# Kernel tuning notes

Measured on AMD Instinct MI355X. Metric: run time of the kernel, lower is better.

Reference implementation:

```python
import jax, jax.numpy as jnp
import numpy as np

B, D_IN, D_FEAT, N_EX, N_LAB = 4096, 512, 512, 20000, 100
P_FACTOR = 3.0
EPS = 1e-12  # torch F.normalize eps


def setup_inputs() -> dict:
    key = jax.random.key(0)
    k1, k2, k3, k4 = jax.random.split(key, 4)
    features = jax.random.normal(k1, (B, D_IN), dtype=jnp.float32)
    g_weight = jax.random.normal(k2, (D_FEAT, D_IN), dtype=jnp.float32) * (1.0 / np.sqrt(D_IN))
    ex_features = jax.random.normal(k3, (N_EX, D_IN), dtype=jnp.float32)
    ex_classes = jax.random.uniform(k4, (N_EX, N_LAB), dtype=jnp.float32)
    class_reps = jnp.eye(N_LAB, dtype=jnp.float32)  # one_hot(arange(num_labels)) since class_dim is None
    return {"features": features, "g_weight": g_weight, "ex_features": ex_features,
            "ex_classes": ex_classes, "class_reps": class_reps}


def _l2_normalize(x):
    n = jnp.linalg.norm(x, axis=-1, keepdims=True)
    return x / jnp.maximum(n, EPS)


def _l1_normalize(x):
    n = jnp.sum(jnp.abs(x), axis=-1, keepdims=True)
    return x / jnp.maximum(n, EPS)


def reference(features, g_weight, ex_features, ex_classes, class_reps):
    # g projection (bias-free linear)
    f = features @ g_weight.T          # [B, D_FEAT]
    e = ex_features @ g_weight.T       # [N_EX, D_FEAT]
    # exemplar class representations
    ex_class_reps = _l1_normalize(ex_classes) @ class_reps  # [N_EX, N_LAB]
    # cosine similarity
    s = _l2_normalize(f) @ _l2_normalize(e).T  # [B, N_EX]
    # power-sign activation then L1 row-normalize
    a = jnp.sign(s) * jnp.abs(s) ** P_FACTOR
    a = _l1_normalize(a)
    echo = a @ ex_class_reps           # [B, N_LAB]
    return echo
```

## Files before the change

kernel.cpp:

```cpp
#include <hip/hip_runtime.h>

#define B_ROWS 4096
#define D      512
#define N_EX   20000
#define EXP2   20096
#define MPROJ  24192
#define N_LAB  100
#define LABP2  128
#define NT2    157
#define SPLITS 16

typedef __attribute__((ext_vector_type(8)))  short short8v;
typedef __attribute__((ext_vector_type(16))) float f32x16;
typedef __attribute__((ext_vector_type(2)))  int   int2v;
typedef unsigned short u16;

__device__ __forceinline__ u16 f2bf(float x) {
    unsigned u = __builtin_bit_cast(unsigned, x);
    u = u + 0x7FFFu + ((u >> 16) & 1u);
    return (u16)(u >> 16);
}
__device__ __forceinline__ float bf2f(u16 h) {
    unsigned u = ((unsigned)h) << 16;
    return __builtin_bit_cast(float, u);
}

__device__ __forceinline__ void gload16(const void* g, void* l) {
    __builtin_amdgcn_global_load_lds((const __attribute__((address_space(1))) void*)g,
                                     (__attribute__((address_space(3))) void*)l, 16, 0, 0);
}

__device__ __forceinline__ unsigned pk_bf16(float a, float b) {
    unsigned r;
    asm("v_cvt_pk_bf16_f32 %0, %1, %2" : "=v"(r) : "v"(a), "v"(b));
    return r;
}

__device__ __forceinline__ void swap_halves(unsigned &a, unsigned &b) {
#if __has_builtin(__builtin_amdgcn_permlane32_swap)
    int2v r = __builtin_amdgcn_permlane32_swap((int)a, (int)b, false, false);
    a = (unsigned)r[0]; b = (unsigned)r[1];
#else
    unsigned sa = (unsigned)__shfl_xor((int)a, 32, 64);
    unsigned sb = (unsigned)__shfl_xor((int)b, 32, 64);
    if (threadIdx.x & 32) a = sb; else b = sa;
#endif
}

#define MFMA32(a, b, c) __builtin_amdgcn_mfma_f32_32x32x16_bf16((a), (b), (c), 0, 0, 0)

__global__ __launch_bounds__(256)
void split3_k(const float* __restrict__ f, const float* __restrict__ ex,
              const float* __restrict__ gw, u16* __restrict__ xall,
              u16* __restrict__ wh) {
    int i8 = blockIdx.x * 256 + threadIdx.x;
    int row = i8 >> 6;
    int e = (i8 & 63) * 8;
    const float* src = nullptr;
    u16* dst;
    if (row < B_ROWS) {
        src = &f[(size_t)row * D + e];
        dst = &xall[(size_t)row * D + e];
    } else if (row < B_ROWS + EXP2) {
        int er = row - B_ROWS;
        if (er < N_EX) src = &ex[(size_t)er * D + e];
        dst = &xall[(size_t)row * D + e];
    } else if (row < B_ROWS + EXP2 + D) {
        int wr = row - B_ROWS - EXP2;
        src = &gw[(size_t)wr * D + e];
        dst = &wh[(size_t)wr * D + e];
    } else return;
    short8v h = {0,0,0,0,0,0,0,0};
    if (src) {
        float4 a = *(const float4*)src, b = *(const float4*)(src + 4);
        float v[8] = {a.x,a.y,a.z,a.w,b.x,b.y,b.z,b.w};
        #pragma unroll
        for (int j = 0; j < 8; ++j) h[j] = (short)f2bf(v[j]);
    }
    *(short8v*)dst = h;
}

__global__ __launch_bounds__(512, 4)
void gemm128_k(const u16* __restrict__ A, const u16* __restrict__ B,
               u16* __restrict__ C) {
    __shared__ u16 BUF[2][128][128];
    const int tid = threadIdx.x;
    const int l = tid & 63, w = tid >> 6;
    const int wa = w >> 2, wb = w & 3;
    const int l31 = l & 31, l5 = l >> 5;
    const int m0 = blockIdx.x * 128, n0 = blockIdx.y * 128;
    const int qrow_in = l >> 4;
    const int gs = l & 15;

    f32x16 sacc[2] = {};

    auto STAGE = [&](int nx, int kc_) {
        const int kofs = kc_ * 64;
        #pragma unroll
        for (int i = 0; i < 4; ++i) {
            const int q = w * 4 + i;
            const int r = q * 4 + qrow_in;
            const int g = gs ^ (r & 15);
            const u16* src = (g < 8)
                ? &A[(size_t)(m0 + r) * D + kofs + g * 8]
                : &B[(size_t)(n0 + r) * D + kofs + (g - 8) * 8];
            gload16(src, (u16*)&BUF[nx][0][0] + q * 512);
        }
    };

    STAGE(0, 0);
    __syncthreads();
    int cur = 0;
    for (int kc = 0; kc < 8; ++kc) {
        if (kc < 7) STAGE(cur ^ 1, kc + 1);
        const u16* base = &BUF[cur][0][0];
        #pragma unroll
        for (int ks = 0; ks < 4; ++ks) {
            const int gk = ks * 2 + l5;
            short8v aX[2], bW;
            #pragma unroll
            for (int ei = 0; ei < 2; ++ei) {
                int r = wa * 64 + ei * 32 + l31;
                aX[ei] = *(const short8v*)(base + r * 128 + (gk ^ (r & 15)) * 8);
            }
            {
                int r = wb * 32 + l31;
                bW = *(const short8v*)(base + r * 128 + ((gk | 8) ^ (r & 15)) * 8);
            }
            sacc[0] = MFMA32(aX[0], bW, sacc[0]);
            sacc[1] = MFMA32(aX[1], bW, sacc[1]);
        }
        __syncthreads();
        cur ^= 1;
    }
    #pragma unroll
    for (int ei = 0; ei < 2; ++ei)
        #pragma unroll
        for (int r = 0; r < 16; ++r) {
            int row = m0 + wa * 64 + ei * 32 + (r & 3) + 8 * (r >> 2) + 4 * l5;
            int col = n0 + wb * 32 + l31;
            C[(size_t)row * D + col] = f2bf(sacc[ei][r]);
        }
}

__global__ __launch_bounds__(256)
void inve3_k(const u16* __restrict__ enh, float* __restrict__ inve3) {
    const int row = blockIdx.x * 4 + (threadIdx.x >> 6);
    const int ln = threadIdx.x & 63;
    if (row >= EXP2) return;
    short8v hv = *(const short8v*)&enh[(size_t)row * D + ln * 8];
    float ss = 0.f;
    #pragma unroll
    for (int j = 0; j < 8; ++j) { float v = bf2f((u16)hv[j]); ss += v * v; }
    #pragma unroll
    for (int off = 32; off > 0; off >>= 1) ss += __shfl_xor(ss, off, 64);
    if (ln == 0) {
        float q = (ss > 0.f) ? rsqrtf(ss) : 0.f;
        inve3[row] = q * q * q;
    }
}

__global__ __launch_bounds__(256)
void ecrT_k(const float* __restrict__ exc, const float* __restrict__ creps,
            u16* __restrict__ th) {
    __shared__ float CRT[N_LAB][101];
    __shared__ float EX[128][N_LAB];
    __shared__ float INV[128];
    __shared__ u16 OUT[LABP2][128];
    const int tid = threadIdx.x;
    const int e0 = blockIdx.x * 128;
    for (int i = tid; i < N_LAB * N_LAB; i += 256) {
        int c = i / N_LAB, lab = i % N_LAB;
        CRT[lab][c] = creps[i];
    }
    for (int i = tid; i < 128 * N_LAB; i += 256) {
        int el = i / N_LAB, c = i % N_LAB;
        int e = e0 + el;
        EX[el][c] = (e < N_EX) ? exc[(size_t)e * N_LAB + c] : 0.f;
    }
    __syncthreads();
    if (tid < 128) {
        float s = 0.f;
        for (int c = 0; c < N_LAB; ++c) s += fabsf(EX[tid][c]);
        INV[tid] = 1.0f / fmaxf(s, 1e-12f);
    }
    __syncthreads();
    const int lab = tid & 127;
    for (int el = tid >> 7; el < 128; el += 2) {
        float acc = 0.f;
        if (lab < N_LAB) {
            #pragma unroll 4
            for (int c = 0; c < N_LAB; ++c) acc += EX[el][c] * CRT[lab][c];
            acc *= INV[el];
        }
        OUT[lab][el] = f2bf(acc);
    }
    __syncthreads();
    for (int i = tid; i < LABP2 * 16; i += 256) {
        int lb = i >> 4, ch = i & 15;
        *(short8v*)&th[(size_t)lb * EXP2 + e0 + ch * 8] = *(const short8v*)&OUT[lb][ch * 8];
    }
}

__global__ __launch_bounds__(512, 2)
void fused_k(const u16* __restrict__ fnh, const u16* __restrict__ enh,
             const u16* __restrict__ ecth, const float* __restrict__ inve3,
             float* __restrict__ nump, float* __restrict__ denp2) {
    __shared__ u16 SMEM[65536];
    u16* ENR = SMEM;
    u16* FNR = SMEM + 16384;
    u16* WTB = SMEM + 49152;

    const int tid = threadIdx.x;
    const int l = tid & 63, w = tid >> 6;
    const int we = w >> 2, wq = w & 3;
    const int l31 = l & 31, l5 = l >> 5;
    const int wg = blockIdx.x;
    const int split = (wg & 7) + 8 * ((wg >> 3) & 1);
    const int m0 = (wg >> 4) * 256;

    union FragU { short8v s; unsigned u[4]; };

    f32x16 num_acc[2][4] = {};
    float den_th[2] = {0.f, 0.f};

    auto STAGE_AB = [&](int nx, int t_, int kc_) {
        const int e0_ = t_ * 128, kofs = kc_ * 64;
        #pragma unroll
        for (int i = 0; i < 2; ++i) {
            const int p = w * 128 + i * 64 + l;
            const int line = p >> 4, q = (p & 15) ^ (line & 15);
            const int row = line * 2 + (q >> 3), g = q & 7;
            gload16(&enh[(size_t)(e0_ + row) * D + kofs + g * 8],
                    ENR + nx * 8192 + p * 8);
        }
        #pragma unroll
        for (int i = 0; i < 4; ++i) {
            const int p = w * 256 + i * 64 + l;
            const int line = p >> 4, q = (p & 15) ^ (line & 15);
            const int row = line * 2 + (q >> 3), g = q & 7;
            gload16(&fnh[(size_t)(m0 + row) * D + kofs + g * 8],
                    FNR + nx * 16384 + p * 8);
        }
    };
    auto STAGE_WT = [&](int t_) {
        const int e0_ = t_ * 128;
        #pragma unroll
        for (int i = 0; i < 4; ++i) {
            const int p = w * 256 + i * 64 + l;
            const int lab = p >> 4, g = p & 15;
            gload16(&ecth[(size_t)lab * EXP2 + e0_ + ((g ^ (lab & 15)) * 8)],
                    WTB + p * 8);
        }
    };
    auto ldfrag = [&](const u16* base, int r, int gk) -> short8v {
        int line = r >> 1;
        int slot = (((r & 1) << 3) | gk) ^ (line & 15);
        return *(const short8v*)(base + line * 128 + slot * 8);
    };

    STAGE_AB(0, split, 0);
    int cur = 0;

    for (int t = split; t < NT2; t += SPLITS) {
        const int e0 = t * 128;
        f32x16 sacc[2][2] = {};
        for (int kc = 0; kc < 8; ++kc) {
            if (kc < 7) {
                STAGE_AB(cur ^ 1, t, kc + 1);
                asm volatile("s_waitcnt vmcnt(6)" ::: "memory");
            } else {
                STAGE_WT(t);
                asm volatile("s_waitcnt vmcnt(4)" ::: "memory");
            }
            __builtin_amdgcn_s_barrier();
            const u16* eb = ENR + cur * 8192;
            const u16* fb = FNR + cur * 16384;
            #pragma unroll
            for (int ks = 0; ks < 4; ++ks) {
                const int gk = ks * 2 + l5;
                short8v aE[2], bF[2];
                #pragma unroll
                for (int ei = 0; ei < 2; ++ei)
                    aE[ei] = ldfrag(eb, we * 64 + ei * 32 + l31, gk);
                #pragma unroll
                for (int mi = 0; mi < 2; ++mi)
                    bF[mi] = ldfrag(fb, wq * 64 + mi * 32 + l31, gk);
                #pragma unroll
                for (int ei = 0; ei < 2; ++ei)
                    #pragma unroll
                    for (int mi = 0; mi < 2; ++mi)
                        sacc[ei][mi] = MFMA32(aE[ei], bF[mi], sacc[ei][mi]);
            }
            asm volatile("s_waitcnt lgkmcnt(0)" ::: "memory");
            __builtin_amdgcn_s_barrier();
            if (kc < 7) cur ^= 1;
        }
        const int tn = t + SPLITS;
        if (tn < NT2) {
            STAGE_AB(cur ^ 1, tn, 0);
            asm volatile("s_waitcnt vmcnt(6)" ::: "memory");
        } else {
            asm volatile("s_waitcnt vmcnt(0)" ::: "memory");
        }
        __builtin_amdgcn_s_barrier();
        #pragma unroll
        for (int ei = 0; ei < 2; ++ei) {
            float iv[16];
            #pragma unroll
            for (int r = 0; r < 16; ++r)
                iv[r] = inve3[e0 + we * 64 + ei * 32 + (r & 3) + 8 * (r >> 2) + 4 * l5];
            FragU fr[2][2];
            #pragma unroll
            for (int mi = 0; mi < 2; ++mi) {
                float a3[16];
                #pragma unroll
                for (int r = 0; r < 16; ++r) {
                    float sv = sacc[ei][mi][r];
                    float c3 = sv * sv * sv * iv[r];
                    a3[r] = c3;
                    den_th[mi] += fabsf(c3);
                }
                #pragma unroll
                for (int c = 0; c < 2; ++c) {
                    unsigned p01 = pk_bf16(a3[c*8+0], a3[c*8+1]);
                    unsigned p23 = pk_bf16(a3[c*8+2], a3[c*8+3]);
                    unsigned p45 = pk_bf16(a3[c*8+4], a3[c*8+5]);
                    unsigned p67 = pk_bf16(a3[c*8+6], a3[c*8+7]);
                    swap_halves(p01, p45);
                    swap_halves(p23, p67);
                    fr[mi][c].u[0] = p01; fr[mi][c].u[1] = p23;
                    fr[mi][c].u[2] = p45; fr[mi][c].u[3] = p67;
                }
            }
            #pragma unroll
            for (int c = 0; c < 2; ++c) {
                const int gw2 = (we * 4 + ei * 2 + c) * 2 + l5;
                #pragma unroll
                for (int lt = 0; lt < 4; ++lt) {
                    int row = lt * 32 + l31;
                    short8v wf = *(const short8v*)(WTB + row * 128 + (gw2 ^ (row & 15)) * 8);
                    num_acc[0][lt] = MFMA32(fr[0][c].s, wf, num_acc[0][lt]);
                    num_acc[1][lt] = MFMA32(fr[1][c].s, wf, num_acc[1][lt]);
                }
            }
        }
        asm volatile("s_waitcnt lgkmcnt(0)" ::: "memory");
        __builtin_amdgcn_s_barrier();
        cur ^= 1;
    }

    #pragma unroll
    for (int mi = 0; mi < 2; ++mi) {
        float v = den_th[mi];
        v += __shfl_xor(v, 32, 64);
        if (l5 == 0)
            denp2[((size_t)split * 2 + we) * B_ROWS + m0 + wq * 64 + mi * 32 + l31] = v;
    }

    float* SMf = (float*)SMEM;
    __syncthreads();
    #pragma unroll
    for (int half = 0; half < 2; ++half) {
        if (we == 1 && (wq >> 1) == half) {
            #pragma unroll
            for (int mi = 0; mi < 2; ++mi)
                #pragma unroll
                for (int lt = 0; lt < 4; ++lt)
                    #pragma unroll
                    for (int r = 0; r < 16; ++r) {
                        int rowf = (r & 3) + 8 * (r >> 2) + 4 * l5;
                        int lrow = (wq & 1) * 64 + mi * 32 + rowf;
                        SMf[lrow * 128 + lt * 32 + l31] = num_acc[mi][lt][r];
                    }
        }
        __syncthreads();
        if (we == 0 && (wq >> 1) == half) {
            #pragma unroll
            for (int mi = 0; mi < 2; ++mi)
                #pragma unroll
                for (int lt = 0; lt < 4; ++lt)
                    #pragma unroll
                    for (int r = 0; r < 16; ++r) {
                        int rowf = (r & 3) + 8 * (r >> 2) + 4 * l5;
                        int lrow = (wq & 1) * 64 + mi * 32 + rowf;
                        float v = num_acc[mi][lt][r] + SMf[lrow * 128 + lt * 32 + l31];
                        int m = m0 + wq * 64 + mi * 32 + rowf;
                        nump[((size_t)split * B_ROWS + m) * LABP2 + lt * 32 + l31] = v;
                    }
        }
        __syncthreads();
    }
}

__global__ __launch_bounds__(128)
void finalize_k(const float* __restrict__ nump, const float* __restrict__ denp2,
                float* __restrict__ out) {
    const int row = blockIdx.x, tid = threadIdx.x;
    float den = 0.f;
    for (int s = 0; s < 2 * SPLITS; ++s)
        den += denp2[(size_t)s * B_ROWS + row];
    if (tid < N_LAB) {
        float acc = 0.f;
        for (int s = 0; s < SPLITS; ++s)
            acc += nump[((size_t)s * B_ROWS + row) * LABP2 + tid];
        out[(size_t)row * N_LAB + tid] = acc / fmaxf(den, 1e-12f);
    }
}

extern "C" void kernel_launch(void* const* d_in, const int* in_sizes, int n_in,
                              void* d_out, int out_size, void* d_ws, size_t ws_size,
                              hipStream_t stream) {
    (void)in_sizes; (void)n_in; (void)out_size; (void)ws_size;
    const float* features    = (const float*)d_in[0];
    const float* g_weight    = (const float*)d_in[1];
    const float* ex_features = (const float*)d_in[2];
    const float* ex_classes  = (const float*)d_in[3];
    const float* class_reps  = (const float*)d_in[4];
    float* out = (float*)d_out;

    size_t off = 0;
    auto alloc = [&](size_t bytes) {
        void* p = (char*)d_ws + off;
        off += (bytes + 255) & ~(size_t)255;
        return p;
    };
    u16* fnh = (u16*)alloc((size_t)B_ROWS * D * 2);
    u16* enh = (u16*)alloc((size_t)EXP2 * D * 2);
    u16* ecth = (u16*)alloc((size_t)LABP2 * EXP2 * 2);
    u16* wh  = (u16*)alloc((size_t)D * D * 2);
    float* inve3 = (float*)alloc((size_t)EXP2 * 4);
    float* nump  = (float*)alloc((size_t)SPLITS * B_ROWS * LABP2 * 4);
    float* denp2 = (float*)alloc((size_t)2 * SPLITS * B_ROWS * 4);
    u16* xall = (u16*)nump;

    const int tot_rows = B_ROWS + EXP2 + D;
    split3_k<<<(tot_rows * 64 + 255) / 256, 256, 0, stream>>>(
        features, ex_features, g_weight, xall, wh);
    gemm128_k<<<dim3(MPROJ / 128, 4), 512, 0, stream>>>(xall, wh, fnh);
    inve3_k<<<(EXP2 + 3) / 4, 256, 0, stream>>>(enh, inve3);
    ecrT_k<<<NT2, 256, 0, stream>>>(ex_classes, class_reps, ecth);
    fused_k<<<256, 512, 0, stream>>>(fnh, enh, ecth, inve3, nump, denp2);
    finalize_k<<<B_ROWS, 128, 0, stream>>>(nump, denp2, out);
}
```

Before: 391.2 us.

## Halve fused kernel block tile and share one double-buffered LDS region

The fused similarity/echo kernel now uses 256-thread blocks covering 128 query rows instead of 512 threads covering 256 rows, and launches twice as many blocks. The E/F tiles and the class-weight tile share a single 64KB double buffer instead of separate regions totalling 128KB, so two blocks can fit per CU. Manual vmcnt/lgkmcnt waits with raw barriers are replaced by plain __syncthreads. The trade-off is that each exemplar tile is now loaded by twice as many blocks, and the coarser sync may reduce load/compute overlap.

```diff
diff --git a/kernel.cpp b/kernel.cpp
--- a/kernel.cpp
+++ b/kernel.cpp
@@ -202,22 +202,18 @@
     }
 }
 
-__global__ __launch_bounds__(512, 2)
+__global__ __launch_bounds__(256, 2)
 void fused_k(const u16* __restrict__ fnh, const u16* __restrict__ enh,
              const u16* __restrict__ ecth, const float* __restrict__ inve3,
              float* __restrict__ nump, float* __restrict__ denp2) {
-    __shared__ u16 SMEM[65536];
-    u16* ENR = SMEM;
-    u16* FNR = SMEM + 16384;
-    u16* WTB = SMEM + 49152;
-
+    __shared__ u16 BUF[2][16384];
     const int tid = threadIdx.x;
     const int l = tid & 63, w = tid >> 6;
-    const int we = w >> 2, wq = w & 3;
+    const int we = w >> 1, wq = w & 1;
     const int l31 = l & 31, l5 = l >> 5;
     const int wg = blockIdx.x;
     const int split = (wg & 7) + 8 * ((wg >> 3) & 1);
-    const int m0 = (wg >> 4) * 256;
+    const int m0 = (wg >> 4) * 128;
 
     union FragU { short8v s; unsigned u[4]; };
 
@@ -227,12 +223,12 @@
     auto STAGE_AB = [&](int nx, int t_, int kc_) {
         const int e0_ = t_ * 128, kofs = kc_ * 64;
         #pragma unroll
-        for (int i = 0; i < 2; ++i) {
-            const int p = w * 128 + i * 64 + l;
+        for (int i = 0; i < 4; ++i) {
+            const int p = w * 256 + i * 64 + l;
             const int line = p >> 4, q = (p & 15) ^ (line & 15);
             const int row = line * 2 + (q >> 3), g = q & 7;
             gload16(&enh[(size_t)(e0_ + row) * D + kofs + g * 8],
-                    ENR + nx * 8192 + p * 8);
+                    BUF[nx] + p * 8);
         }
         #pragma unroll
         for (int i = 0; i < 4; ++i) {
@@ -240,17 +236,17 @@
             const int line = p >> 4, q = (p & 15) ^ (line & 15);
             const int row = line * 2 + (q >> 3), g = q & 7;
             gload16(&fnh[(size_t)(m0 + row) * D + kofs + g * 8],
-                    FNR + nx * 16384 + p * 8);
+                    BUF[nx] + 8192 + p * 8);
         }
     };
-    auto STAGE_WT = [&](int t_) {
+    auto STAGE_WT = [&](int nx, int t_) {
         const int e0_ = t_ * 128;
         #pragma unroll
-        for (int i = 0; i < 4; ++i) {
-            const int p = w * 256 + i * 64 + l;
+        for (int i = 0; i < 8; ++i) {
+            const int p = w * 512 + i * 64 + l;
             const int lab = p >> 4, g = p & 15;
             gload16(&ecth[(size_t)lab * EXP2 + e0_ + ((g ^ (lab & 15)) * 8)],
-                    WTB + p * 8);
+                    BUF[nx] + p * 8);
         }
     };
     auto ldfrag = [&](const u16* base, int r, int gk) -> short8v {
@@ -260,22 +256,17 @@
     };
 
     STAGE_AB(0, split, 0);
+    __syncthreads();
     int cur = 0;
 
     for (int t = split; t < NT2; t += SPLITS) {
         const int e0 = t * 128;
         f32x16 sacc[2][2] = {};
         for (int kc = 0; kc < 8; ++kc) {
-            if (kc < 7) {
-                STAGE_AB(cur ^ 1, t, kc + 1);
-                asm volatile("s_waitcnt vmcnt(6)" ::: "memory");
-            } else {
-                STAGE_WT(t);
-                asm volatile("s_waitcnt vmcnt(4)" ::: "memory");
-            }
-            __builtin_amdgcn_s_barrier();
-            const u16* eb = ENR + cur * 8192;
-            const u16* fb = FNR + cur * 16384;
+            if (kc < 7) STAGE_AB(cur ^ 1, t, kc + 1);
+            else        STAGE_WT(cur ^ 1, t);
+            const u16* eb = BUF[cur];
+            const u16* fb = BUF[cur] + 8192;
             #pragma unroll
             for (int ks = 0; ks < 4; ++ks) {
                 const int gk = ks * 2 + l5;
@@ -292,18 +283,12 @@
                     for (int mi = 0; mi < 2; ++mi)
                         sacc[ei][mi] = MFMA32(aE[ei], bF[mi], sacc[ei][mi]);
             }
-            asm volatile("s_waitcnt lgkmcnt(0)" ::: "memory");
-            __builtin_amdgcn_s_barrier();
-            if (kc < 7) cur ^= 1;
+            __syncthreads();
+            cur ^= 1;
         }
         const int tn = t + SPLITS;
-        if (tn < NT2) {
-            STAGE_AB(cur ^ 1, tn, 0);
-            asm volatile("s_waitcnt vmcnt(6)" ::: "memory");
-        } else {
-            asm volatile("s_waitcnt vmcnt(0)" ::: "memory");
-        }
-        __builtin_amdgcn_s_barrier();
+        if (tn < NT2) STAGE_AB(cur ^ 1, tn, 0);
+        const u16* wb = BUF[cur];
         #pragma unroll
         for (int ei = 0; ei < 2; ++ei) {
             float iv[16];
@@ -339,14 +324,13 @@
                 #pragma unroll
                 for (int lt = 0; lt < 4; ++lt) {
                     int row = lt * 32 + l31;
-                    short8v wf = *(const short8v*)(WTB + row * 128 + (gw2 ^ (row & 15)) * 8);
+                    short8v wf = *(const short8v*)(wb + row * 128 + (gw2 ^ (row & 15)) * 8);
                     num_acc[0][lt] = MFMA32(fr[0][c].s, wf, num_acc[0][lt]);
                     num_acc[1][lt] = MFMA32(fr[1][c].s, wf, num_acc[1][lt]);
                 }
             }
         }
-        asm volatile("s_waitcnt lgkmcnt(0)" ::: "memory");
-        __builtin_amdgcn_s_barrier();
+        __syncthreads();
         cur ^= 1;
     }
 
@@ -358,38 +342,34 @@
             denp2[((size_t)split * 2 + we) * B_ROWS + m0 + wq * 64 + mi * 32 + l31] = v;
     }
 
-    float* SMf = (float*)SMEM;
-    __syncthreads();
-    #pragma unroll
-    for (int half = 0; half < 2; ++half) {
-        if (we == 1 && (wq >> 1) == half) {
-            #pragma unroll
-            for (int mi = 0; mi < 2; ++mi)
-                #pragma unroll
-                for (int lt = 0; lt < 4; ++lt)
-                    #pragma unroll
-                    for (int r = 0; r < 16; ++r) {
-                        int rowf = (r & 3) + 8 * (r >> 2) + 4 * l5;
-                        int lrow = (wq & 1) * 64 + mi * 32 + rowf;
-                        SMf[lrow * 128 + lt * 32 + l31] = num_acc[mi][lt][r];
-                    }
-        }
-        __syncthreads();
-        if (we == 0 && (wq >> 1) == half) {
-            #pragma unroll
-            for (int mi = 0; mi < 2; ++mi)
-                #pragma unroll
-                for (int lt = 0; lt < 4; ++lt)
-                    #pragma unroll
-                    for (int r = 0; r < 16; ++r) {
-                        int rowf = (r & 3) + 8 * (r >> 2) + 4 * l5;
-                        int lrow = (wq & 1) * 64 + mi * 32 + rowf;
-                        float v = num_acc[mi][lt][r] + SMf[lrow * 128 + lt * 32 + l31];
-                        int m = m0 + wq * 64 + mi * 32 + rowf;
-                        nump[((size_t)split * B_ROWS + m) * LABP2 + lt * 32 + l31] = v;
-                    }
-        }
-        __syncthreads();
+    float* SMf = (float*)&BUF[0][0];
+    __syncthreads();
+    if (we == 1) {
+        #pragma unroll
+        for (int mi = 0; mi < 2; ++mi)
+            #pragma unroll
+            for (int lt = 0; lt < 4; ++lt)
+                #pragma unroll
+                for (int r = 0; r < 16; ++r) {
+                    int rowf = (r & 3) + 8 * (r >> 2) + 4 * l5;
+                    int lrow = wq * 64 + mi * 32 + rowf;
+                    SMf[lrow * 128 + lt * 32 + l31] = num_acc[mi][lt][r];
+                }
+    }
+    __syncthreads();
+    if (we == 0) {
+        #pragma unroll
+        for (int mi = 0; mi < 2; ++mi)
+            #pragma unroll
+            for (int lt = 0; lt < 4; ++lt)
+                #pragma unroll
+                for (int r = 0; r < 16; ++r) {
+                    int rowf = (r & 3) + 8 * (r >> 2) + 4 * l5;
+                    int lrow = wq * 64 + mi * 32 + rowf;
+                    float v = num_acc[mi][lt][r] + SMf[lrow * 128 + lt * 32 + l31];
+                    int m = m0 + wq * 64 + mi * 32 + rowf;
+                    nump[((size_t)split * B_ROWS + m) * LABP2 + lt * 32 + l31] = v;
+                }
     }
 }
 
@@ -440,6 +420,6 @@
     gemm128_k<<<dim3(MPROJ / 128, 4), 512, 0, stream>>>(xall, wh, fnh);
     inve3_k<<<(EXP2 + 3) / 4, 256, 0, stream>>>(enh, inve3);
     ecrT_k<<<NT2, 256, 0, stream>>>(ex_classes, class_reps, ecth);
-    fused_k<<<256, 512, 0, stream>>>(fnh, enh, ecth, inve3, nump, denp2);
+    fused_k<<<512, 256, 0, stream>>>(fnh, enh, ecth, inve3, nump, denp2);
     finalize_k<<<B_ROWS, 128, 0, stream>>>(nump, denp2, out);
 }
```

After: 401.3 us. +2.6%, slower.

## Triple-buffer LDS staging to prefetch two K-chunks ahead in fused kernel

Applied to the files above, without the earlier changes.

Replaces the double-buffered E/F staging plus a separate weight buffer with three rotating 48KB LDS slots, so global loads for chunk kc+2 are issued before computing chunk kc. The WT tile reuses slot 2 during the last chunk, and the next tile's first two chunks are prefetched across the epilogue. This aims to hide global-memory latency better and removes one barrier per K step. The cost is a fixed LDS footprint of 144KB with tighter slot-reuse and vmcnt bookkeeping, and the unrolled K loop grows code size.

```diff
diff --git a/kernel.cpp b/kernel.cpp
--- a/kernel.cpp
+++ b/kernel.cpp
@@ -206,10 +206,7 @@
 void fused_k(const u16* __restrict__ fnh, const u16* __restrict__ enh,
              const u16* __restrict__ ecth, const float* __restrict__ inve3,
              float* __restrict__ nump, float* __restrict__ denp2) {
-    __shared__ u16 SMEM[65536];
-    u16* ENR = SMEM;
-    u16* FNR = SMEM + 16384;
-    u16* WTB = SMEM + 49152;
+    __shared__ u16 RB[3][24576];
 
     const int tid = threadIdx.x;
     const int l = tid & 63, w = tid >> 6;
@@ -224,7 +221,7 @@
     f32x16 num_acc[2][4] = {};
     float den_th[2] = {0.f, 0.f};
 
-    auto STAGE_AB = [&](int nx, int t_, int kc_) {
+    auto STAGE_AB = [&](int slot, int t_, int kc_) {
         const int e0_ = t_ * 128, kofs = kc_ * 64;
         #pragma unroll
         for (int i = 0; i < 2; ++i) {
@@ -232,7 +229,7 @@
             const int line = p >> 4, q = (p & 15) ^ (line & 15);
             const int row = line * 2 + (q >> 3), g = q & 7;
             gload16(&enh[(size_t)(e0_ + row) * D + kofs + g * 8],
-                    ENR + nx * 8192 + p * 8);
+                    RB[slot] + p * 8);
         }
         #pragma unroll
         for (int i = 0; i < 4; ++i) {
@@ -240,7 +237,7 @@
             const int line = p >> 4, q = (p & 15) ^ (line & 15);
             const int row = line * 2 + (q >> 3), g = q & 7;
             gload16(&fnh[(size_t)(m0 + row) * D + kofs + g * 8],
-                    FNR + nx * 16384 + p * 8);
+                    RB[slot] + 8192 + p * 8);
         }
     };
     auto STAGE_WT = [&](int t_) {
@@ -250,7 +247,7 @@
             const int p = w * 256 + i * 64 + l;
             const int lab = p >> 4, g = p & 15;
             gload16(&ecth[(size_t)lab * EXP2 + e0_ + ((g ^ (lab & 15)) * 8)],
-                    WTB + p * 8);
+                    RB[2] + p * 8);
         }
     };
     auto ldfrag = [&](const u16* base, int r, int gk) -> short8v {
@@ -258,52 +255,65 @@
         int slot = (((r & 1) << 3) | gk) ^ (line & 15);
         return *(const short8v*)(base + line * 128 + slot * 8);
     };
+    auto COMPUTE = [&](const u16* base, f32x16 (&sacc)[2][2]) {
+        const u16* eb = base;
+        const u16* fb = base + 8192;
+        #pragma unroll
+        for (int ks = 0; ks < 4; ++ks) {
+            const int gk = ks * 2 + l5;
+            short8v aE[2], bF[2];
+            #pragma unroll
+            for (int ei = 0; ei < 2; ++ei)
+                aE[ei] = ldfrag(eb, we * 64 + ei * 32 + l31, gk);
+            #pragma unroll
+            for (int mi = 0; mi < 2; ++mi)
+                bF[mi] = ldfrag(fb, wq * 64 + mi * 32 + l31, gk);
+            #pragma unroll
+            for (int ei = 0; ei < 2; ++ei)
+                #pragma unroll
+                for (int mi = 0; mi < 2; ++mi)
+                    sacc[ei][mi] = MFMA32(aE[ei], bF[mi], sacc[ei][mi]);
+        }
+    };
 
     STAGE_AB(0, split, 0);
-    int cur = 0;
+    STAGE_AB(1, split, 1);
+    asm volatile("s_waitcnt vmcnt(6)" ::: "memory");
+    __builtin_amdgcn_s_barrier();
 
     for (int t = split; t < NT2; t += SPLITS) {
         const int e0 = t * 128;
+        const int tn = t + SPLITS;
+        const bool hasnext = (tn < NT2);
         f32x16 sacc[2][2] = {};
-        for (int kc = 0; kc < 8; ++kc) {
-            if (kc < 7) {
-                STAGE_AB(cur ^ 1, t, kc + 1);
-                asm volatile("s_waitcnt vmcnt(6)" ::: "memory");
-            } else {
-                STAGE_WT(t);
-                asm volatile("s_waitcnt vmcnt(4)" ::: "memory");
-            }
+
+        #pragma unroll
+        for (int kc = 0; kc < 6; ++kc) {
+            STAGE_AB((kc + 2) % 3, t, kc + 2);
+            COMPUTE(RB[kc % 3], sacc);
+            asm volatile("s_waitcnt lgkmcnt(0)" ::: "memory");
+            asm volatile("s_waitcnt vmcnt(6)" ::: "memory");
             __builtin_amdgcn_s_barrier();
-            const u16* eb = ENR + cur * 8192;
-            const u16* fb = FNR + cur * 16384;
-            #pragma unroll
-            for (int ks = 0; ks < 4; ++ks) {
-                const int gk = ks * 2 + l5;
-                short8v aE[2], bF[2];
-                #pragma unroll
-                for (int ei = 0; ei < 2; ++ei)
-                    aE[ei] = ldfrag(eb, we * 64 + ei * 32 + l31, gk);
-                #pragma unroll
-                for (int mi = 0; mi < 2; ++mi)
-                    bF[mi] = ldfrag(fb, wq * 64 + mi * 32 + l31, gk);
-                #pragma unroll
-                for (int ei = 0; ei < 2; ++ei)
-                    #pragma unroll
-                    for (int mi = 0; mi < 2; ++mi)
-                        sacc[ei][mi] = MFMA32(aE[ei], bF[mi], sacc[ei][mi]);
-            }
+        }
+        STAGE_WT(t);
+        COMPUTE(RB[0], sacc);
+        asm volatile("s_waitcnt lgkmcnt(0)" ::: "memory");
+        asm volatile("s_waitcnt vmcnt(4)" ::: "memory");
+        __builtin_amdgcn_s_barrier();
+        if (hasnext) {
+            STAGE_AB(0, tn, 0);
+            COMPUTE(RB[1], sacc);
             asm volatile("s_waitcnt lgkmcnt(0)" ::: "memory");
-            __builtin_amdgcn_s_barrier();
-            if (kc < 7) cur ^= 1;
-        }
-        const int tn = t + SPLITS;
-        if (tn < NT2) {
-            STAGE_AB(cur ^ 1, tn, 0);
             asm volatile("s_waitcnt vmcnt(6)" ::: "memory");
         } else {
+            COMPUTE(RB[1], sacc);
+            asm volatile("s_waitcnt lgkmcnt(0)" ::: "memory");
             asm volatile("s_waitcnt vmcnt(0)" ::: "memory");
         }
         __builtin_amdgcn_s_barrier();
+
+        if (hasnext) STAGE_AB(1, tn, 1);
+        const u16* wb = RB[2];
         #pragma unroll
         for (int ei = 0; ei < 2; ++ei) {
             float iv[16];
@@ -339,15 +349,16 @@
                 #pragma unroll
                 for (int lt = 0; lt < 4; ++lt) {
                     int row = lt * 32 + l31;
-                    short8v wf = *(const short8v*)(WTB + row * 128 + (gw2 ^ (row & 15)) * 8);
+                    short8v wf = *(const short8v*)(wb + row * 128 + (gw2 ^ (row & 15)) * 8);
                     num_acc[0][lt] = MFMA32(fr[0][c].s, wf, num_acc[0][lt]);
                     num_acc[1][lt] = MFMA32(fr[1][c].s, wf, num_acc[1][lt]);
                 }
             }
         }
         asm volatile("s_waitcnt lgkmcnt(0)" ::: "memory");
+        if (hasnext) asm volatile("s_waitcnt vmcnt(6)" ::: "memory");
+        else         asm volatile("s_waitcnt vmcnt(0)" ::: "memory");
         __builtin_amdgcn_s_barrier();
-        cur ^= 1;
     }
 
     #pragma unroll
@@ -358,7 +369,7 @@
             denp2[((size_t)split * 2 + we) * B_ROWS + m0 + wq * 64 + mi * 32 + l31] = v;
     }
 
-    float* SMf = (float*)SMEM;
+    float* SMf = (float*)&RB[0][0];
     __syncthreads();
     #pragma unroll
     for (int half = 0; half < 2; ++half) {
```

Result: slower. 543.9 us (+39.0%).
